# Kernel optimization log

Measured on AMD Instinct MI355X. Metric: run time of the kernel, lower is better.

Reference implementation:

```python
import jax, jax.numpy as jnp
import numpy as np

N = 100000   # nodes
E = 1600000  # edges (avg degree 16)
D = 64       # in_dim
H = 64       # hidden_dim
NEG_SLOPE = 0.2


def setup_inputs() -> dict:
    key = jax.random.key(0)
    ks = jax.random.split(key, 10)
    s = 0.1  # param init scale
    return {
        "x": jax.random.normal(ks[0], (N, D), jnp.float32),
        "edge_index": jax.random.randint(ks[1], (2, E), 0, N, dtype=jnp.int64),
        "h": jax.random.normal(ks[2], (1, N, H), jnp.float32),
        "c": jax.random.normal(ks[3], (1, N, H), jnp.float32),
        "W_gat": jax.random.normal(ks[4], (D, H), jnp.float32) * s,
        "att_src": jax.random.normal(ks[5], (H,), jnp.float32) * s,
        "att_dst": jax.random.normal(ks[6], (H,), jnp.float32) * s,
        "bias_gat": jax.random.normal(ks[7], (H,), jnp.float32) * s,
        "W_ih": jax.random.normal(ks[8], (4 * H, H), jnp.float32) * s,
        "W_hh": jax.random.normal(ks[9], (4 * H, H), jnp.float32) * s,
    }


def reference(x, edge_index, h, c, W_gat, att_src, att_dst, bias_gat, W_ih, W_hh):
    src, dst = edge_index[0], edge_index[1]  # message j -> i

    # ---- Breadth: GATConv (heads=1) + tanh ----
    xs = x @ W_gat                             # [N, H] projected features
    a_src = xs @ att_src                       # [N]
    a_dst = xs @ att_dst                       # [N]
    e = jax.nn.leaky_relu(a_src[src] + a_dst[dst], NEG_SLOPE)  # [E]
    # scatter-softmax over incoming edges of each destination node
    m = jax.lax.stop_gradient(jax.ops.segment_max(e, dst, num_segments=N))
    p = jnp.exp(e - m[dst])
    z = jax.ops.segment_sum(p, dst, num_segments=N)
    alpha = p / (z[dst] + 1e-16)               # [E]
    agg = jax.ops.segment_sum(xs[src] * alpha[:, None], dst, num_segments=N)
    xb = jnp.tanh(agg + bias_gat)              # [N, H]

    # ---- Depth: single-step bias-free LSTM ----
    h0, c0 = h[0], c[0]                        # [N, H]
    gates = xb @ W_ih.T + h0 @ W_hh.T          # [N, 4H]
    i, f, g, o = jnp.split(gates, 4, axis=-1)  # torch gate order i,f,g,o
    c1 = jax.nn.sigmoid(f) * c0 + jax.nn.sigmoid(i) * jnp.tanh(g)
    h1 = jax.nn.sigmoid(o) * jnp.tanh(c1)
    return h1, h1[None], c1[None]
```

## Files before the change

kernel.cpp:

```cpp
#include <hip/hip_runtime.h>
#include <cmath>

#define NN 100000
#define EE 1600000
#define NB 1563
#define CAP 1344
#define EPB 25
#define NTILE 6250
#define PROJB 1563
#define CVTB 3125

using bf16x8 = __attribute__((ext_vector_type(8))) __bf16;
using f32x4  = __attribute__((ext_vector_type(4))) float;

__device__ __forceinline__ unsigned short f2bf(float f) {
  __bf16 b = (__bf16)f;
  return __builtin_bit_cast(unsigned short, b);
}
__device__ __forceinline__ float bflo(unsigned int u) {
  return __uint_as_float(u << 16);
}
__device__ __forceinline__ float bfhi(unsigned int u) {
  return __uint_as_float(u & 0xffff0000u);
}
__device__ __forceinline__ float sigmoidf_(float v) {
  return 1.0f / (1.0f + __expf(-v));
}
__device__ __forceinline__ float tanhfast(float v) {
  return 1.0f - 2.0f / (1.0f + __expf(2.0f * v));
}
__device__ __forceinline__ bf16x8 cvt8(float4 a, float4 b) {
  bf16x8 r;
  r[0]=(__bf16)a.x; r[1]=(__bf16)a.y; r[2]=(__bf16)a.z; r[3]=(__bf16)a.w;
  r[4]=(__bf16)b.x; r[5]=(__bf16)b.y; r[6]=(__bf16)b.z; r[7]=(__bf16)b.w;
  return r;
}

__global__ __launch_bounds__(128) void k_prep(
    const float* __restrict__ Wih, const float* __restrict__ Whh,
    const float* __restrict__ Wg,
    unsigned short* __restrict__ wperm, unsigned short* __restrict__ wgp)
{
  if (blockIdx.x < 256) {
    const int p = blockIdx.x, k = threadIdx.x;
    const int g = p & 3;
    const int h = (p >> 4) + ((p >> 2) & 3) * 16;
    const int row = g*64 + h;
    const float v = (k < 64) ? Wih[row*64 + k] : Whh[row*64 + (k - 64)];
    const int gp = (k >> 3) ^ (p & 15);
    wperm[p*128 + gp*8 + (k & 7)] = f2bf(v);
  } else {
    for (int idx = threadIdx.x; idx < 4096; idx += 128) {
      const int lane = idx >> 6, r = idx & 63;
      const int nt = r >> 4, kf = (r >> 3) & 1, j = r & 7;
      const int m = lane & 15, quad = lane >> 4;
      wgp[idx] = f2bf(Wg[(kf*32 + quad*8 + j)*64 + nt*16 + m]);
    }
  }
}

__global__ __launch_bounds__(256) void k_binproj(
    const int* __restrict__ ei, int* __restrict__ bcursor,
    unsigned int* __restrict__ binned,
    const float* __restrict__ x, const unsigned short* __restrict__ wgp,
    const float* __restrict__ att_s, const float* __restrict__ att_d,
    unsigned short* __restrict__ xs16, float* __restrict__ a_src,
    float* __restrict__ a_dst,
    const float* __restrict__ h0, unsigned short* __restrict__ h16)
{
  if (blockIdx.x < 256) {
    __shared__ int cnt[NB];
    __shared__ int gbase[NB];
    const int tid = threadIdx.x;
    const size_t base = (size_t)blockIdx.x * 256 * EPB;

    for (int b = tid; b < NB; b += 256) cnt[b] = 0;
    __syncthreads();

    unsigned int pay[EPB];
    int bidx[EPB], pos[EPB];
    #pragma unroll
    for (int j = 0; j < EPB; ++j) {
      const size_t e = base + (size_t)j*256 + tid;
      if (e < EE) {
        const int s = ei[e];
        const int d = ei[EE + e];
        bidx[j] = d >> 6;
        pay[j] = (unsigned)s | ((unsigned)(d & 63) << 17);
        pos[j] = atomicAdd(&cnt[bidx[j]], 1);
      } else {
        bidx[j] = -1;
      }
    }
    __syncthreads();

    for (int b = tid; b < NB; b += 256) {
      const int c = cnt[b];
      gbase[b] = c ? atomicAdd(&bcursor[b*16], c) : 0;
    }
    __syncthreads();

    #pragma unroll
    for (int j = 0; j < EPB; ++j) {
      if (bidx[j] >= 0) {
        const int g = gbase[bidx[j]] + pos[j];
        if (g < CAP) binned[(size_t)bidx[j]*CAP + g] = pay[j];
      }
    }
  } else if (blockIdx.x < 256 + PROJB) {
    const int lane = threadIdx.x & 63;
    const int wave = threadIdx.x >> 6;
    const int tile = (blockIdx.x - 256) * 4 + wave;
    if (tile >= NTILE) return;
    const int m = lane & 15, quad = lane >> 4;

    bf16x8 bfrag[4][2];
    {
      const unsigned short* wp = wgp + lane*64;
      #pragma unroll
      for (int nt = 0; nt < 4; ++nt)
        #pragma unroll
        for (int kf = 0; kf < 2; ++kf)
          bfrag[nt][kf] = *(const bf16x8*)(wp + nt*16 + kf*8);
    }

    const int row = tile*16 + m;
    bf16x8 afrag[2];
    #pragma unroll
    for (int kf = 0; kf < 2; ++kf) {
      const float4* p = (const float4*)(x + (size_t)row*64 + kf*32 + quad*8);
      afrag[kf] = cvt8(p[0], p[1]);
    }

    f32x4 acc[4];
    #pragma unroll
    for (int nt = 0; nt < 4; ++nt) acc[nt] = f32x4{0.f, 0.f, 0.f, 0.f};
    #pragma unroll
    for (int nt = 0; nt < 4; ++nt)
      #pragma unroll
      for (int kf = 0; kf < 2; ++kf)
        acc[nt] = __builtin_amdgcn_mfma_f32_16x16x32_bf16(
            afrag[kf], bfrag[nt][kf], acc[nt], 0, 0, 0);

    float ss[4] = {0.f,0.f,0.f,0.f}, sd[4] = {0.f,0.f,0.f,0.f};
    #pragma unroll
    for (int nt = 0; nt < 4; ++nt) {
      const float av = att_s[nt*16 + m], dv = att_d[nt*16 + m];
      #pragma unroll
      for (int r = 0; r < 4; ++r) {
        const float v = acc[nt][r];
        xs16[(size_t)(tile*16 + quad*4 + r)*64 + nt*16 + m] = f2bf(v);
        ss[r] += v * av;
        sd[r] += v * dv;
      }
    }
    #pragma unroll
    for (int off = 1; off < 16; off <<= 1) {
      #pragma unroll
      for (int r = 0; r < 4; ++r) {
        ss[r] += __shfl_xor(ss[r], off);
        sd[r] += __shfl_xor(sd[r], off);
      }
    }
    if (m == 0) {
      #pragma unroll
      for (int r = 0; r < 4; ++r) {
        a_src[tile*16 + quad*4 + r] = ss[r];
        a_dst[tile*16 + quad*4 + r] = sd[r];
      }
    }
  } else {
    const int idx = (blockIdx.x - 256 - PROJB)*256 + threadIdx.x;
    const float* p = h0 + (size_t)idx*8;
    const bf16x8 v = cvt8(*(const float4*)p, *(const float4*)(p + 4));
    *(bf16x8*)(h16 + (size_t)idx*8) = v;
  }
}

__global__ __launch_bounds__(256) void k_agg(
    const int* __restrict__ bcursor, const unsigned int* __restrict__ binned,
    const float* __restrict__ a_src, const float* __restrict__ a_dst,
    const unsigned short* __restrict__ xs16, const float* __restrict__ bias,
    unsigned short* __restrict__ xb16)
{
  __shared__ uint2 raw2[CAP];
  __shared__ uint2 csre[CAP];
  __shared__ float zsum[64], invzsh[64], adsh[64];
  __shared__ int cnt[64], offs[64], cursor[64];
  const int b = blockIdx.x;
  const int tid = threadIdx.x;
  const int ne = min(bcursor[b*16], CAP);

  if (tid < 64) {
    cnt[tid] = 0;
    zsum[tid] = 0.f;
    const int node = b*64 + tid;
    adsh[tid] = (node < NN) ? a_dst[node] : 0.f;
  }
  __syncthreads();

  for (int i = tid; i < ne; i += 256) {
    const unsigned int w = binned[(size_t)b*CAP + i];
    const int s = (int)(w & 0x1FFFFu);
    const int dl = (int)((w >> 17) & 63u);
    float ev = a_src[s] + adsh[dl];
    ev = (ev >= 0.f) ? ev : 0.2f*ev;
    const float pv = __expf(ev);
    raw2[i] = make_uint2(w, __float_as_uint(pv));
    atomicAdd(&cnt[dl], 1);
    atomicAdd(&zsum[dl], pv);
  }
  __syncthreads();

  if (tid < 64) {
    const int v = cnt[tid];
    int inc = v;
    #pragma unroll
    for (int dd = 1; dd < 64; dd <<= 1) {
      const int o = __shfl_up(inc, dd, 64);
      if (tid >= dd) inc += o;
    }
    offs[tid] = inc - v;
    cursor[tid] = inc - v;
    invzsh[tid] = 1.f / (zsum[tid] + 1e-16f);
  }
  __syncthreads();

  for (int i = tid; i < ne; i += 256) {
    const uint2 r = raw2[i];
    const int dl = (int)((r.x >> 17) & 63u);
    const int pos = atomicAdd(&cursor[dl], 1);
    csre[pos] = make_uint2(r.x & 0x1FFFFu, r.y);
  }
  __syncthreads();

  const int lane = tid & 63;
  const int wv = tid >> 6;
  const int grp = lane >> 4, l16 = lane & 15;
  const float4 b4 = *(const float4*)(bias + l16*4);
  const unsigned short* xrow = xs16 + l16*4;
  for (int t = 0; t < 16; ++t) {
    const int nl = wv*16 + t;
    const int node = b*64 + nl;
    if (node >= NN) break;
    const int bse = offs[nl];
    const int dg = cnt[nl];
    float acc0=0.f, acc1=0.f, acc2=0.f, acc3=0.f;
    for (int e = grp; e < dg; e += 4) {
      const uint2 sp = csre[bse + e];
      const float pv = __uint_as_float(sp.y);
      const uint2 rw = *(const uint2*)(xrow + (size_t)sp.x*64);
      acc0 += pv*bflo(rw.x); acc1 += pv*bfhi(rw.x);
      acc2 += pv*bflo(rw.y); acc3 += pv*bfhi(rw.y);
    }
    #pragma unroll
    for (int off = 16; off < 64; off <<= 1) {
      acc0 += __shfl_xor(acc0, off);
      acc1 += __shfl_xor(acc1, off);
      acc2 += __shfl_xor(acc2, off);
      acc3 += __shfl_xor(acc3, off);
    }
    if (lane < 16) {
      const float invz = invzsh[nl];
      ushort4 o;
      o.x = f2bf(tanhfast(acc0*invz + b4.x));
      o.y = f2bf(tanhfast(acc1*invz + b4.y));
      o.z = f2bf(tanhfast(acc2*invz + b4.z));
      o.w = f2bf(tanhfast(acc3*invz + b4.w));
      *(ushort4*)(xb16 + (size_t)node*64 + l16*4) = o;
    }
  }
}

__global__ __launch_bounds__(1024, 2) void k_lstm(
    const unsigned short* __restrict__ xb16, const unsigned short* __restrict__ h16,
    const float* __restrict__ c0, const unsigned short* __restrict__ wperm,
    float* __restrict__ out)
{
  __shared__ unsigned short wlds[256*128];
  const int tid = threadIdx.x;
  {
    const float4* gs = (const float4*)wperm;
    float4* ls = (float4*)wlds;
    #pragma unroll
    for (int i = 0; i < 4; ++i) ls[tid + i*1024] = gs[tid + i*1024];
  }
  __syncthreads();

  const int w = tid >> 6, lane = tid & 63;
  const int wv = w & 3, tsub = w >> 2;
  const int m = lane & 15, quad = lane >> 4;
  const int tile = blockIdx.x*4 + tsub;
  if (tile >= NTILE) return;
  const int node = tile*16 + m;

  bf16x8 bfr[4];
  bfr[0] = *(const bf16x8*)(xb16 + (size_t)node*64 + quad*8);
  bfr[1] = *(const bf16x8*)(xb16 + (size_t)node*64 + 32 + quad*8);
  bfr[2] = *(const bf16x8*)(h16 + (size_t)node*64 + quad*8);
  bfr[3] = *(const bf16x8*)(h16 + (size_t)node*64 + 32 + quad*8);

  const int q32 = (m >> 2) & 3;
  const int base = (wv*64 + m)*256 + ((quad ^ (m & 3)) << 4);
  const char* lb = (const char*)wlds;
  const int a0 = base + ((0 ^ q32) << 6);
  const int a1 = base + ((1 ^ q32) << 6);
  const int a2 = base + ((2 ^ q32) << 6);
  const int a3 = base + ((3 ^ q32) << 6);

  f32x4 acc[4];
  #pragma unroll
  for (int u = 0; u < 4; ++u) acc[u] = f32x4{0.f, 0.f, 0.f, 0.f};
  #pragma unroll
  for (int u = 0; u < 4; ++u) {
    const int uo = u*4096;
    const bf16x8 w0 = *(const bf16x8*)(lb + a0 + uo);
    const bf16x8 w1 = *(const bf16x8*)(lb + a1 + uo);
    const bf16x8 w2 = *(const bf16x8*)(lb + a2 + uo);
    const bf16x8 w3 = *(const bf16x8*)(lb + a3 + uo);
    acc[u] = __builtin_amdgcn_mfma_f32_16x16x32_bf16(w0, bfr[0], acc[u], 0, 0, 0);
    acc[u] = __builtin_amdgcn_mfma_f32_16x16x32_bf16(w1, bfr[1], acc[u], 0, 0, 0);
    acc[u] = __builtin_amdgcn_mfma_f32_16x16x32_bf16(w2, bfr[2], acc[u], 0, 0, 0);
    acc[u] = __builtin_amdgcn_mfma_f32_16x16x32_bf16(w3, bfr[3], acc[u], 0, 0, 0);
  }

  const size_t obase = (size_t)node*64 + quad*16 + wv*4;
  const float4 cv = *(const float4*)(c0 + obase);
  const float cvv[4] = {cv.x, cv.y, cv.z, cv.w};
  float h1a[4], c1a[4];
  #pragma unroll
  for (int u = 0; u < 4; ++u) {
    const float gi = acc[u][0], gf = acc[u][1];
    const float gg = acc[u][2], go = acc[u][3];
    const float c1 = sigmoidf_(gf)*cvv[u] + sigmoidf_(gi)*tanhfast(gg);
    h1a[u] = sigmoidf_(go)*tanhfast(c1);
    c1a[u] = c1;
  }
  const float4 hv  = make_float4(h1a[0], h1a[1], h1a[2], h1a[3]);
  const float4 c1v = make_float4(c1a[0], c1a[1], c1a[2], c1a[3]);
  *(float4*)(out + obase) = hv;
  *(float4*)(out + (size_t)NN*64 + obase) = hv;
  *(float4*)(out + (size_t)2*NN*64 + obase) = c1v;
}

extern "C" void kernel_launch(void* const* d_in, const int* in_sizes, int n_in,
                              void* d_out, int out_size, void* d_ws, size_t ws_size,
                              hipStream_t stream) {
  const float* x    = (const float*)d_in[0];
  const int*   ei   = (const int*)d_in[1];
  const float* h    = (const float*)d_in[2];
  const float* c    = (const float*)d_in[3];
  const float* Wg   = (const float*)d_in[4];
  const float* atts = (const float*)d_in[5];
  const float* attd = (const float*)d_in[6];
  const float* bg   = (const float*)d_in[7];
  const float* Wih  = (const float*)d_in[8];
  const float* Whh  = (const float*)d_in[9];
  float* out = (float*)d_out;

  char* w = (char*)d_ws;
  unsigned short* xs16  = (unsigned short*)w; w += (size_t)NN*64*2;
  unsigned short* xb16  = (unsigned short*)w; w += (size_t)NN*64*2;
  unsigned short* h16   = (unsigned short*)w; w += (size_t)NN*64*2;
  unsigned short* wperm = (unsigned short*)w; w += (size_t)256*128*2;
  unsigned short* wgp   = (unsigned short*)w; w += (size_t)4096*2;
  unsigned int*   binned= (unsigned int*)w;  w += (size_t)NB*CAP*4;
  float* a_src = (float*)w; w += (size_t)NN*4;
  float* a_dst = (float*)w; w += (size_t)NN*4;
  int* bcursor = (int*)w;   w += (size_t)NB*16*4;

  hipMemsetAsync(bcursor, 0, (size_t)NB*16*4, stream);

  k_prep    <<<257, 128, 0, stream>>>(Wih, Whh, Wg, wperm, wgp);
  k_binproj <<<256 + PROJB + CVTB, 256, 0, stream>>>(
      ei, bcursor, binned, x, wgp, atts, attd, xs16, a_src, a_dst, h, h16);
  k_agg     <<<NB, 256, 0, stream>>>(bcursor, binned, a_src, a_dst, xs16, bg, xb16);
  k_lstm    <<<PROJB, 1024, 0, stream>>>(xb16, h16, c, wperm, out);
}
```

Before: 289.4 us.

## Sort in-block edges by destination and source bucket for gather locality

Replaces the per-destination counting sort in the aggregation kernel with a 4096-key counting sort over (destination, source>>11) buckets. Counts are packed as 16-bit pairs, and the prefix sum runs block-wide with a wave scan. The aim is to make each node's neighbour gathers from xs16 more address-ordered, which should improve cache locality. It also batches the binned and a_src loads into unrolled registers so more memory requests are in flight. In exchange it adds a larger shared-memory histogram and scan, and it re-reads the binned array from global memory in the scatter pass.

```diff
diff --git a/kernel.cpp b/kernel.cpp
--- a/kernel.cpp
+++ b/kernel.cpp
@@ -183,54 +183,105 @@
     const unsigned short* __restrict__ xs16, const float* __restrict__ bias,
     unsigned short* __restrict__ xb16)
 {
-  __shared__ uint2 raw2[CAP];
+  __shared__ unsigned int parray[CAP];
   __shared__ uint2 csre[CAP];
+  __shared__ unsigned int cnt[2048];
   __shared__ float zsum[64], invzsh[64], adsh[64];
-  __shared__ int cnt[64], offs[64], cursor[64];
+  __shared__ int base64[64], deg64[64];
+  __shared__ unsigned int wtot[4];
   const int b = blockIdx.x;
   const int tid = threadIdx.x;
   const int ne = min(bcursor[b*16], CAP);
 
+  for (int i = tid; i < 2048; i += 256) cnt[i] = 0;
   if (tid < 64) {
-    cnt[tid] = 0;
     zsum[tid] = 0.f;
     const int node = b*64 + tid;
     adsh[tid] = (node < NN) ? a_dst[node] : 0.f;
   }
   __syncthreads();
 
-  for (int i = tid; i < ne; i += 256) {
-    const unsigned int w = binned[(size_t)b*CAP + i];
-    const int s = (int)(w & 0x1FFFFu);
-    const int dl = (int)((w >> 17) & 63u);
-    float ev = a_src[s] + adsh[dl];
-    ev = (ev >= 0.f) ? ev : 0.2f*ev;
-    const float pv = __expf(ev);
-    raw2[i] = make_uint2(w, __float_as_uint(pv));
-    atomicAdd(&cnt[dl], 1);
-    atomicAdd(&zsum[dl], pv);
+  {
+    unsigned int w6[6];
+    float as6[6];
+    #pragma unroll
+    for (int k = 0; k < 6; ++k) {
+      const int i = tid + k*256;
+      w6[k] = (i < ne) ? binned[(size_t)b*CAP + i] : 0u;
+    }
+    #pragma unroll
+    for (int k = 0; k < 6; ++k) {
+      const int i = tid + k*256;
+      as6[k] = (i < ne) ? a_src[w6[k] & 0x1FFFFu] : 0.f;
+    }
+    #pragma unroll
+    for (int k = 0; k < 6; ++k) {
+      const int i = tid + k*256;
+      if (i < ne) {
+        const unsigned int s = w6[k] & 0x1FFFFu;
+        const int dl = (int)((w6[k] >> 17) & 63u);
+        float ev = as6[k] + adsh[dl];
+        ev = (ev >= 0.f) ? ev : 0.2f*ev;
+        const float pv = __expf(ev);
+        parray[i] = __float_as_uint(pv);
+        const int key = dl*64 + (int)(s >> 11);
+        atomicAdd(&cnt[key >> 1], (key & 1) ? 0x10000u : 1u);
+        atomicAdd(&zsum[dl], pv);
+      }
+    }
+  }
+  __syncthreads();
+
+  {
+    unsigned int loc[8];
+    unsigned int sum = 0;
+    #pragma unroll
+    for (int j = 0; j < 8; ++j) {
+      loc[j] = cnt[tid*8 + j];
+      sum += (loc[j] & 0xffffu) + (loc[j] >> 16);
+    }
+    const int lane = tid & 63, wv = tid >> 6;
+    unsigned int run = sum;
+    #pragma unroll
+    for (int off = 1; off < 64; off <<= 1) {
+      const unsigned int o = __shfl_up(run, off, 64);
+      if (lane >= off) run += o;
+    }
+    if (lane == 63) wtot[wv] = run;
+    __syncthreads();
+    unsigned int wbase = 0;
+    for (int w2 = 0; w2 < wv; ++w2) wbase += wtot[w2];
+    unsigned int ex = wbase + run - sum;
+    #pragma unroll
+    for (int j = 0; j < 8; ++j) {
+      const unsigned int lo = loc[j] & 0xffffu, hi = loc[j] >> 16;
+      cnt[tid*8 + j] = ex | ((ex + lo) << 16);
+      ex += lo + hi;
+    }
   }
   __syncthreads();
 
   if (tid < 64) {
-    const int v = cnt[tid];
-    int inc = v;
-    #pragma unroll
-    for (int dd = 1; dd < 64; dd <<= 1) {
-      const int o = __shfl_up(inc, dd, 64);
-      if (tid >= dd) inc += o;
-    }
-    offs[tid] = inc - v;
-    cursor[tid] = inc - v;
+    const int b0 = (int)(cnt[(tid*64) >> 1] & 0xffffu);
+    const int e0 = (tid == 63) ? ne : (int)(cnt[((tid+1)*64) >> 1] & 0xffffu);
+    base64[tid] = b0;
+    deg64[tid] = e0 - b0;
     invzsh[tid] = 1.f / (zsum[tid] + 1e-16f);
   }
   __syncthreads();
 
-  for (int i = tid; i < ne; i += 256) {
-    const uint2 r = raw2[i];
-    const int dl = (int)((r.x >> 17) & 63u);
-    const int pos = atomicAdd(&cursor[dl], 1);
-    csre[pos] = make_uint2(r.x & 0x1FFFFu, r.y);
+  #pragma unroll
+  for (int k = 0; k < 6; ++k) {
+    const int i = tid + k*256;
+    if (i < ne) {
+      const unsigned int w = binned[(size_t)b*CAP + i];
+      const unsigned int s = w & 0x1FFFFu;
+      const int dl = (int)((w >> 17) & 63u);
+      const int key = dl*64 + (int)(s >> 11);
+      const unsigned int old = atomicAdd(&cnt[key >> 1], (key & 1) ? 0x10000u : 1u);
+      const int pos = (int)((key & 1) ? (old >> 16) : (old & 0xffffu));
+      csre[pos] = make_uint2(s, parray[i]);
+    }
   }
   __syncthreads();
 
@@ -243,8 +294,8 @@
     const int nl = wv*16 + t;
     const int node = b*64 + nl;
     if (node >= NN) break;
-    const int bse = offs[nl];
-    const int dg = cnt[nl];
+    const int bse = base64[nl];
+    const int dg = deg64[nl];
     float acc0=0.f, acc1=0.f, acc2=0.f, acc3=0.f;
     for (int e = grp; e < dg; e += 4) {
       const uint2 sp = csre[bse + e];
```

Measured after the change: 316.8 us. 1.09x slower.
